# Optimization experiments

Measured on AMD Instinct MI355X. Metric: run time of the kernel, lower is better.

The kernel has to match this reference:

```python
import jax, jax.numpy as jnp
import numpy as np

B, C, L = 32, 128, 4096          # batch, n_channels, signal length
P, Q = 100, 20                   # n_projections, n_quantiles


def setup_inputs() -> dict:
    key = jax.random.key(0)
    k1, k2, k3, k4 = jax.random.split(key, 4)
    X = jax.random.normal(k1, (B, C, L), dtype=jnp.float32)
    # conv1d kernel of shape (P, C, 1) collapsed to (P, C)
    W = jax.random.normal(k2, (P, C), dtype=jnp.float32)
    s = 2.33 * jnp.sqrt(jnp.float32(C))
    min_vals = -s + 0.1 * jax.random.normal(k3, (P,), dtype=jnp.float32)
    max_vals = s + 0.1 * jax.random.normal(k4, (P,), dtype=jnp.float32)
    return {"X": X, "W": W, "min_vals": min_vals, "max_vals": max_vals}


def reference(X, W, min_vals, max_vals):
    # kernel-size-1 conv1d == channel projection
    a = jnp.einsum('bcl,pc->bpl', X, W)  # [B, P, L]
    fracs = jnp.arange(1, Q + 1, dtype=a.dtype) / jnp.asarray(Q + 1, a.dtype)
    thr = min_vals[None, :] + (max_vals - min_vals)[None, :] * fracs[:, None]  # [Q, P]

    def body(carry, t):  # t: [P] thresholds for one quantile
        cdf_q = jnp.mean((a < t[None, :, None]).astype(a.dtype), axis=-1)  # [B, P]
        return carry, cdf_q

    _, cdf = jax.lax.scan(body, None, thr)          # [Q, B, P]
    cdf = jnp.transpose(cdf, (1, 2, 0))             # [B, P, Q]
    return cdf.reshape(B, P * Q)
```

## Files before the change

kernel.cpp:

```cpp
#include <hip/hip_runtime.h>
#include <hip/hip_bf16.h>

#define B_   32
#define C_   128
#define L_   4096
#define P_   100
#define PT   112
#define NPT  7
#define Q_   20
#define NBIN 21
#define WROW 136

typedef short  bf16x8 __attribute__((ext_vector_type(8)));
typedef float  f32x4  __attribute__((ext_vector_type(4)));

__device__ inline unsigned short f2bf(float f) {
    __hip_bfloat16 h = __float2bfloat16(f);
    unsigned short u; __builtin_memcpy(&u, &h, 2);
    return u;
}

__global__ __launch_bounds__(256, 4)
void radon_mfma_kernel(const float* __restrict__ X, const float* __restrict__ W,
                       const float* __restrict__ minv, const float* __restrict__ maxv,
                       float* __restrict__ out) {
    __shared__ unsigned short Wlds[PT * WROW];
    __shared__ int   hist[P_ * NBIN];
    __shared__ float mn_s[P_], invd_s[P_];

    const int tid  = threadIdx.x;
    const int b    = blockIdx.y;
    const int lblk = blockIdx.x;
    const int wave = tid >> 6;
    const int lane = tid & 63;
    const int quad = lane >> 4;
    const int nn   = lane & 15;

    for (int i = tid; i < PT * (C_ / 2); i += 256) {
        const int row = i / (C_ / 2);
        const int cp  = (i - row * (C_ / 2)) * 2;
        float2 w2 = make_float2(0.f, 0.f);
        if (row < P_) w2 = *(const float2*)(W + row * C_ + cp);
        const unsigned int pk = (unsigned int)f2bf(w2.x) | ((unsigned int)f2bf(w2.y) << 16);
        *(unsigned int*)(&Wlds[row * WROW + cp]) = pk;
    }
    for (int i = tid; i < P_; i += 256) {
        const float mn = minv[i];
        mn_s[i]   = mn;
        invd_s[i] = (float)NBIN / (maxv[i] - mn);
    }
    for (int i = tid; i < P_ * NBIN; i += 256) hist[i] = 0;
    __syncthreads();

    const int l0 = lblk * 128 + wave * 32;
    const float* Xb = X + (size_t)b * C_ * L_;
    bf16x8 bfrag[2][4];
#pragma unroll
    for (int lt = 0; lt < 2; ++lt) {
        const int l = l0 + lt * 16 + nn;
#pragma unroll
        for (int ks = 0; ks < 4; ++ks) {
            float xv[8];
#pragma unroll
            for (int j = 0; j < 8; ++j)
                xv[j] = Xb[(size_t)(ks * 32 + quad * 8 + j) * L_ + l];
            bf16x8 f;
#pragma unroll
            for (int j = 0; j < 8; ++j) f[j] = (short)f2bf(xv[j]);
            bfrag[lt][ks] = f;
        }
    }

    for (int pt = 0; pt < NPT; ++pt) {
        const int p0 = pt * 16;
        bf16x8 afrag[4];
#pragma unroll
        for (int ks = 0; ks < 4; ++ks)
            afrag[ks] = *(const bf16x8*)(&Wlds[(p0 + nn) * WROW + ks * 32 + quad * 8]);

        f32x4 acc0 = {0.f, 0.f, 0.f, 0.f};
        f32x4 acc1 = {0.f, 0.f, 0.f, 0.f};
#pragma unroll
        for (int ks = 0; ks < 4; ++ks) {
            acc0 = __builtin_amdgcn_mfma_f32_16x16x32_bf16(afrag[ks], bfrag[0][ks], acc0, 0, 0, 0);
            acc1 = __builtin_amdgcn_mfma_f32_16x16x32_bf16(afrag[ks], bfrag[1][ks], acc1, 0, 0, 0);
        }

#pragma unroll
        for (int r = 0; r < 4; ++r) {
            const int p = p0 + quad * 4 + r;
            if (p < P_) {
                const float mn = mn_s[p], invd = invd_s[p];
                {
                    const float t = (acc0[r] - mn) * invd;
                    int k = 0;
                    if (t > 0.f) { const int ki = (int)t; k = (ki > 20) ? 20 : ki; }
                    atomicAdd(&hist[p * NBIN + k], 1);
                }
                {
                    const float t = (acc1[r] - mn) * invd;
                    int k = 0;
                    if (t > 0.f) { const int ki = (int)t; k = (ki > 20) ? 20 : ki; }
                    atomicAdd(&hist[p * NBIN + k], 1);
                }
            }
        }
    }
    __syncthreads();

    for (int i = tid; i < P_ * Q_; i += 256) {
        const int p  = i / Q_;
        const int qi = i - p * Q_;
        int s = 0;
        for (int k = 0; k <= qi; ++k) s += hist[p * NBIN + k];
        atomicAdd(&out[((size_t)b * P_ + p) * Q_ + qi], (float)s * (1.0f / (float)L_));
    }
}

extern "C" void kernel_launch(void* const* d_in, const int* in_sizes, int n_in,
                              void* d_out, int out_size, void* d_ws, size_t ws_size,
                              hipStream_t stream) {
    const float* X  = (const float*)d_in[0];
    const float* W  = (const float*)d_in[1];
    const float* mn = (const float*)d_in[2];
    const float* mx = (const float*)d_in[3];
    float* out = (float*)d_out;

    hipMemsetAsync(out, 0, (size_t)out_size * sizeof(float), stream);

    dim3 grid(L_ / 128, B_);
    radon_mfma_kernel<<<grid, dim3(256), 0, stream>>>(X, W, mn, mx, out);
}
```

Measured before the change: 114.6 us.

## Pre-pack bf16 weights in fragment order and overlap X loads with LDS setup

A small prep kernel converts W to bf16 once, laid out in MFMA fragment order in the workspace. Each block then fills LDS with straight 16-byte copies instead of converting fp32 weights on every block. The X global loads are issued before the weight copy and histogram init, so their latency overlaps that setup, and the bf16 conversion now packs two values at a time. The cost is an extra kernel launch and more registers held live across the setup code.

```diff
diff --git a/kernel.cpp b/kernel.cpp
--- a/kernel.cpp
+++ b/kernel.cpp
@@ -5,14 +5,15 @@
 #define C_   128
 #define L_   4096
 #define P_   100
-#define PT   112
 #define NPT  7
 #define Q_   20
 #define NBIN 21
-#define WROW 136
+#define NCH  (NPT * 4)
+#define CHS  512
 
-typedef short  bf16x8 __attribute__((ext_vector_type(8)));
-typedef float  f32x4  __attribute__((ext_vector_type(4)));
+typedef short          bf16x8 __attribute__((ext_vector_type(8)));
+typedef float          f32x4  __attribute__((ext_vector_type(4)));
+typedef unsigned short u16x8  __attribute__((ext_vector_type(8)));
 
 __device__ inline unsigned short f2bf(float f) {
     __hip_bfloat16 h = __float2bfloat16(f);
@@ -20,11 +21,25 @@
     return u;
 }
 
+__global__ void prep_w_kernel(const float* __restrict__ W, unsigned short* __restrict__ Wf) {
+    const int t = blockIdx.x * 256 + threadIdx.x;
+    if (t >= NCH * 64) return;
+    const int chunk = t >> 6, lane = t & 63;
+    const int pt = chunk >> 2, ks = chunk & 3;
+    const int p  = pt * 16 + (lane & 15);
+    const int c0 = ks * 32 + (lane >> 4) * 8;
+    u16x8 v;
+#pragma unroll
+    for (int j = 0; j < 8; ++j)
+        v[j] = (p < P_) ? f2bf(W[p * C_ + c0 + j]) : (unsigned short)0;
+    *(u16x8*)(Wf + (size_t)t * 8) = v;
+}
+
 __global__ __launch_bounds__(256, 4)
-void radon_mfma_kernel(const float* __restrict__ X, const float* __restrict__ W,
-                       const float* __restrict__ minv, const float* __restrict__ maxv,
-                       float* __restrict__ out) {
-    __shared__ unsigned short Wlds[PT * WROW];
+void radon_mfma2_kernel(const float* __restrict__ X, const unsigned short* __restrict__ Wf,
+                        const float* __restrict__ minv, const float* __restrict__ maxv,
+                        float* __restrict__ out) {
+    __shared__ unsigned short Wlds[NCH * CHS];
     __shared__ int   hist[P_ * NBIN];
     __shared__ float mn_s[P_], invd_s[P_];
 
@@ -36,13 +51,23 @@
     const int quad = lane >> 4;
     const int nn   = lane & 15;
 
-    for (int i = tid; i < PT * (C_ / 2); i += 256) {
-        const int row = i / (C_ / 2);
-        const int cp  = (i - row * (C_ / 2)) * 2;
-        float2 w2 = make_float2(0.f, 0.f);
-        if (row < P_) w2 = *(const float2*)(W + row * C_ + cp);
-        const unsigned int pk = (unsigned int)f2bf(w2.x) | ((unsigned int)f2bf(w2.y) << 16);
-        *(unsigned int*)(&Wlds[row * WROW + cp]) = pk;
+    const int l0 = lblk * 128 + wave * 32;
+    const float* Xb = X + (size_t)b * C_ * L_;
+    float xv[2][4][8];
+#pragma unroll
+    for (int lt = 0; lt < 2; ++lt)
+#pragma unroll
+        for (int ks = 0; ks < 4; ++ks)
+#pragma unroll
+            for (int j = 0; j < 8; ++j)
+                xv[lt][ks][j] = Xb[(size_t)(ks * 32 + quad * 8 + j) * L_ + l0 + lt * 16 + nn];
+
+    {
+        const int4* src = (const int4*)Wf;
+        int4* dst = (int4*)Wlds;
+#pragma unroll
+        for (int k = 0; k < NCH * 64 / 256; ++k)
+            dst[tid + k * 256] = src[tid + k * 256];
     }
     for (int i = tid; i < P_; i += 256) {
         const float mn = minv[i];
@@ -50,33 +75,28 @@
         invd_s[i] = (float)NBIN / (maxv[i] - mn);
     }
     for (int i = tid; i < P_ * NBIN; i += 256) hist[i] = 0;
+
+    bf16x8 bfrag[2][4];
+#pragma unroll
+    for (int lt = 0; lt < 2; ++lt)
+#pragma unroll
+        for (int ks = 0; ks < 4; ++ks) {
+            unsigned int u[4];
+#pragma unroll
+            for (int jp = 0; jp < 4; ++jp) {
+                __hip_bfloat162 h2 = __float22bfloat162_rn(
+                    make_float2(xv[lt][ks][2 * jp], xv[lt][ks][2 * jp + 1]));
+                __builtin_memcpy(&u[jp], &h2, 4);
+            }
+            __builtin_memcpy(&bfrag[lt][ks], u, 16);
+        }
     __syncthreads();
 
-    const int l0 = lblk * 128 + wave * 32;
-    const float* Xb = X + (size_t)b * C_ * L_;
-    bf16x8 bfrag[2][4];
-#pragma unroll
-    for (int lt = 0; lt < 2; ++lt) {
-        const int l = l0 + lt * 16 + nn;
-#pragma unroll
-        for (int ks = 0; ks < 4; ++ks) {
-            float xv[8];
-#pragma unroll
-            for (int j = 0; j < 8; ++j)
-                xv[j] = Xb[(size_t)(ks * 32 + quad * 8 + j) * L_ + l];
-            bf16x8 f;
-#pragma unroll
-            for (int j = 0; j < 8; ++j) f[j] = (short)f2bf(xv[j]);
-            bfrag[lt][ks] = f;
-        }
-    }
-
     for (int pt = 0; pt < NPT; ++pt) {
-        const int p0 = pt * 16;
         bf16x8 afrag[4];
 #pragma unroll
         for (int ks = 0; ks < 4; ++ks)
-            afrag[ks] = *(const bf16x8*)(&Wlds[(p0 + nn) * WROW + ks * 32 + quad * 8]);
+            afrag[ks] = *(const bf16x8*)(&Wlds[((pt * 4 + ks) * 64 + lane) * 8]);
 
         f32x4 acc0 = {0.f, 0.f, 0.f, 0.f};
         f32x4 acc1 = {0.f, 0.f, 0.f, 0.f};
@@ -88,7 +108,7 @@
 
 #pragma unroll
         for (int r = 0; r < 4; ++r) {
-            const int p = p0 + quad * 4 + r;
+            const int p = pt * 16 + quad * 4 + r;
             if (p < P_) {
                 const float mn = mn_s[p], invd = invd_s[p];
                 {
@@ -125,9 +145,11 @@
     const float* mn = (const float*)d_in[2];
     const float* mx = (const float*)d_in[3];
     float* out = (float*)d_out;
+    unsigned short* Wf = (unsigned short*)d_ws;
 
+    prep_w_kernel<<<NCH * 64 / 256, 256, 0, stream>>>(W, Wf);
     hipMemsetAsync(out, 0, (size_t)out_size * sizeof(float), stream);
 
     dim3 grid(L_ / 128, B_);
-    radon_mfma_kernel<<<grid, dim3(256), 0, stream>>>(X, W, mn, mx, out);
+    radon_mfma2_kernel<<<grid, dim3(256), 0, stream>>>(X, Wf, mn, mx, out);
 }
```

Result: faster. 110.7 us (-3.4%).
